# Optimization experiments

Measured on AMD Instinct MI355X. Metric: run time of the kernel, lower is better.

Reference implementation:

```python
import jax, jax.numpy as jnp
import numpy as np

MB, NK, DM, DT = 4096, 8, 1024, 128
EPS = 1e-3  # LayerNormalization eps, added to sigma OUTSIDE sqrt


def setup_inputs() -> dict:
    key = jax.random.key(0)
    ks = jax.random.split(key, 7)
    xav = lambda fan_in, fan_out: (2.0 / (fan_in + fan_out)) ** 0.5
    return {
        "q": jax.random.normal(ks[0], (MB, NK, DM), jnp.float32),
        "k": jax.random.normal(ks[1], (MB, NK, DM), jnp.float32),
        "v": jax.random.normal(ks[2], (MB, NK, DM), jnp.float32),
        "w_qs": jax.random.normal(ks[3], (NK, DM, DT), jnp.float32) * xav(DM, DT),
        "w_ks": jax.random.normal(ks[4], (NK, DM, DT), jnp.float32) * xav(DM, DT),
        "w_vs": jax.random.normal(ks[5], (NK, DM, DT), jnp.float32) * xav(DM, DT),
        # torch Linear: weight [out, in] = [NK*DM, NK*DT]
        "proj_w": jax.random.normal(ks[6], (NK * DM, NK * DT), jnp.float32) * xav(NK * DT, NK * DM),
        "proj_b": jnp.zeros((NK * DM,), jnp.float32),
        "gamma": jnp.ones((DM,), jnp.float32),
        "beta": jnp.zeros((DM,), jnp.float32),
    }


def reference(q, k, v, w_qs, w_ks, w_vs, proj_w, proj_b, gamma, beta):
    mb, nk, dm = q.shape
    dt = w_qs.shape[-1]
    residual = v

    # torch: q.view(n_kernel, mb, d_model) on contiguous [mb, nk, dm] == raw reshape
    q_s = jnp.einsum('nbd,ndt->nbt', q.reshape(nk, mb, dm), w_qs)  # [nk, mb, dt]
    k_s = jnp.einsum('nbd,ndt->nbt', k.reshape(nk, mb, dm), w_ks)
    v_s = jnp.einsum('nbd,ndt->nbt', v.reshape(nk, mb, dm), w_vs)

    # ScaledDotProductAttention on [nk*mb, 1, dt] -> scores [.,1,1]; softmax over
    # a singleton dim is identically 1, so output == v_s (faithful to source).
    temper = np.float32(np.sqrt(dm))
    scores = jnp.sum(q_s * k_s, axis=-1) / temper            # [nk, mb]
    attn = jax.nn.softmax(scores[:, :, None, None], axis=-1)  # [nk, mb, 1, 1] == 1.0
    out = attn[..., 0] * v_s                                  # [nk, mb, dt]
    attns = attn.reshape(nk * mb, 1, 1)

    # torch .view(mb, nk*dt) on the [nk, mb, dt]-contiguous buffer (raw reshape)
    outputs = out.reshape(mb, nk * dt)
    outputs = outputs @ proj_w.T + proj_b                     # [mb, nk*dm]
    z = outputs.reshape(mb, nk, dm) + residual

    # custom LayerNormalization: unbiased std, eps outside sqrt
    mu = jnp.mean(z, axis=-1, keepdims=True)
    sigma = jnp.std(z, axis=-1, keepdims=True, ddof=1)
    output = (z - mu) / (sigma + EPS) * gamma + beta
    return (output, attns)
```

## Files before the change

### kernel.cpp

```cpp
#include <hip/hip_runtime.h>
#include <cstdint>
#include <cstddef>

#define MB_   4096
#define NK_   8
#define DM_   1024
#define DT_   128

typedef __bf16 bf16;
typedef __bf16 bf16x8 __attribute__((ext_vector_type(8)));
typedef __bf16 bf16x4 __attribute__((ext_vector_type(4)));
typedef float  f32x4  __attribute__((ext_vector_type(4)));

__device__ __forceinline__ void gload_lds16(const void* g, void* l) {
  __builtin_amdgcn_global_load_lds(
      (__attribute__((address_space(1))) void*)g,
      (__attribute__((address_space(3))) void*)l,
      16, 0, 0);
}

__device__ __forceinline__ int hsw(int r) { return (r ^ (r >> 2)) & 3; }

__global__ void prep_kernel(const float* __restrict__ pw, bf16* __restrict__ pwb,
                            const float* __restrict__ wvs, bf16* __restrict__ wvt) {
  int b = blockIdx.x;
  if (b < 8192) {
    size_t i = ((size_t)b * 256 + threadIdx.x) * 4;
    float4 f = *(const float4*)&pw[i];
    bf16x4 o = { (bf16)f.x, (bf16)f.y, (bf16)f.z, (bf16)f.w };
    *(bf16x4*)&pwb[i] = o;
  } else {
    int o = (b - 8192) * 256 + threadIdx.x;
    int d = o & 1023;
    int t = (o >> 10) & 127;
    int n = o >> 17;
    wvt[o] = (bf16)wvs[(size_t)n * 131072 + (size_t)d * 128 + t];
  }
}

__global__ __launch_bounds__(256, 2) void gemm1_kernel(
    const float* __restrict__ vflat, const bf16* __restrict__ WvT,
    bf16* __restrict__ A2)
{
  __shared__ __align__(16) bf16 As[64 * 32];
  __shared__ __align__(16) bf16 Bs[128 * 32];
  const int tid  = threadIdx.x;
  const int wave = tid >> 6, lane = tid & 63;
  const int wm = wave >> 1, wn = wave & 1;
  const int n  = blockIdx.y;
  const int b0 = blockIdx.x * 64;

  const int r  = tid >> 2;
  const int hr = hsw(r);
  const int cs = (tid & 3) ^ hr;

  const float* ag = vflat + ((size_t)(n * MB_ + b0 + r)) * 1024 + (tid & 3) * 8;
  bf16* awr = As + r * 32 + cs * 8;
  const bf16* bg = WvT + (size_t)n * 131072 + (size_t)r * 1024 + cs * 8;
  char* bsb = (char*)Bs + wave * 1024;

  f32x4 acc[2][4] = {};
  const int krow = lane & 15;
  const int cch  = lane >> 4;
  const int swoff = ((cch ^ hsw(krow)) << 4);

  for (int kt = 0; kt < 32; ++kt) {
    const bf16* bptr = bg + kt * 32;
    gload_lds16(bptr,             bsb);
    gload_lds16(bptr + 64 * 1024, bsb + 4096);
    const float* aptr = ag + kt * 32;
    float4 f0 = *(const float4*)(aptr + 0);
    float4 f1 = *(const float4*)(aptr + 4);
    bf16x8 h0 = { (bf16)f0.x, (bf16)f0.y, (bf16)f0.z, (bf16)f0.w,
                  (bf16)f1.x, (bf16)f1.y, (bf16)f1.z, (bf16)f1.w };
    *(bf16x8*)awr = h0;
    __syncthreads();

    bf16x8 af[2], bfr[4];
    #pragma unroll
    for (int i = 0; i < 2; ++i)
      af[i] = *(const bf16x8*)((const char*)As + (wm * 32 + i * 16 + krow) * 64 + swoff);
    #pragma unroll
    for (int j = 0; j < 4; ++j)
      bfr[j] = *(const bf16x8*)((const char*)Bs + (wn * 64 + j * 16 + krow) * 64 + swoff);
    #pragma unroll
    for (int i = 0; i < 2; ++i)
      #pragma unroll
      for (int j = 0; j < 4; ++j)
        acc[i][j] = __builtin_amdgcn_mfma_f32_16x16x32_bf16(af[i], bfr[j], acc[i][j], 0, 0, 0);
    __syncthreads();
  }

  #pragma unroll
  for (int i = 0; i < 2; ++i) {
    #pragma unroll
    for (int j = 0; j < 4; ++j) {
      int t = wn * 64 + j * 16 + (lane & 15);
      #pragma unroll
      for (int rr = 0; rr < 4; ++rr) {
        int b = b0 + wm * 32 + i * 16 + (lane >> 4) * 4 + rr;
        size_t off = ((size_t)(n * 512 + (b >> 3))) * 1024 + (size_t)(b & 7) * 128 + t;
        A2[off] = (bf16)acc[i][j][rr];
      }
    }
  }
}

template<bool ZB>
__global__ __launch_bounds__(512, 2) void gemm2c_kernel(
    const bf16* __restrict__ A2, const bf16* __restrict__ PW,
    const float* __restrict__ pb, void* __restrict__ xoutp)
{
  __shared__ __align__(16) bf16 As[4][8192];
  __shared__ __align__(16) bf16 Bs[4][8192];

  const int tid  = threadIdx.x;
  const int w    = tid >> 6;
  const int lane = tid & 63;
  const int wm   = w >> 2;
  const int wn   = w & 3;

  const int bid   = blockIdx.x;
  const int x     = bid & 7;
  const int local = bid >> 3;
  const int mt    = local & 15;
  const int nt    = x * 4 + (local >> 4);
  const int m0    = mt * 256;
  const int n0    = nt * 256;

  const int rS = tid >> 2;
  const int cS = (tid & 3) ^ hsw(rS);
  const char* aG0 = (const char*)A2 + (size_t)(m0 + rS) * 2048 + cS * 16;
  const char* aG1 = aG0 + (size_t)128 * 2048;
  const char* bG0 = (const char*)PW + (size_t)(n0 + rS) * 2048 + cS * 16;
  const char* bG1 = bG0 + (size_t)128 * 2048;

  #define STAGE(t) { char* dA = (char*)As[(t) & 3] + tid * 16;               \
                     char* dB = (char*)Bs[(t) & 3] + tid * 16;               \
                     gload_lds16(aG0 + (size_t)(t) * 64, dA);                \
                     gload_lds16(aG1 + (size_t)(t) * 64, dA + 8192);         \
                     gload_lds16(bG0 + (size_t)(t) * 64, dB);                \
                     gload_lds16(bG1 + (size_t)(t) * 64, dB + 8192); }

  STAGE(0); STAGE(1); STAGE(2);
  asm volatile("s_waitcnt vmcnt(8)" ::: "memory");
  __builtin_amdgcn_s_barrier();
  __builtin_amdgcn_sched_barrier(0);

  f32x4 acc[8][4] = {};
  const int fr = lane & 15;
  const int g  = lane >> 4;
  const int swoff = ((g ^ hsw(fr)) << 4);
  const int aRd = (wm * 128 + fr) * 64 + swoff;
  const int bRd = (wn * 64  + fr) * 64 + swoff;

  #pragma unroll 1
  for (int s = 0; s < 32; ++s) {
    if (s < 29) STAGE(s + 3);

    const char* pA = (const char*)As[s & 3] + aRd;
    const char* pB = (const char*)Bs[s & 3] + bRd;
    bf16x8 a[8], b[4];
    #pragma unroll
    for (int m = 0; m < 8; ++m) a[m] = *(const bf16x8*)(pA + m * 1024);
    #pragma unroll
    for (int n = 0; n < 4; ++n) b[n] = *(const bf16x8*)(pB + n * 1024);
    #pragma unroll
    for (int m = 0; m < 8; ++m)
      #pragma unroll
      for (int n = 0; n < 4; ++n)
        acc[m][n] = __builtin_amdgcn_mfma_f32_16x16x32_bf16(a[m], b[n], acc[m][n], 0, 0, 0);

    asm volatile("s_waitcnt lgkmcnt(0)" ::: "memory");
    if (s < 29)       { asm volatile("s_waitcnt vmcnt(8)" ::: "memory"); }
    else if (s == 29) { asm volatile("s_waitcnt vmcnt(4)" ::: "memory"); }
    else if (s == 30) { asm volatile("s_waitcnt vmcnt(0)" ::: "memory"); }
    __builtin_amdgcn_s_barrier();
    __builtin_amdgcn_sched_barrier(0);
  }
  #undef STAGE

  #pragma unroll
  for (int m = 0; m < 8; ++m) {
    #pragma unroll
    for (int n = 0; n < 4; ++n) {
      int nn = n0 + wn * 64 + n * 16 + fr;
      float pbn = pb[nn];
      #pragma unroll
      for (int r = 0; r < 4; ++r) {
        int mm = m0 + wm * 128 + m * 16 + g * 4 + r;
        size_t off = (size_t)mm * 8192 + nn;
        float val = acc[m][n][r] + pbn;
        if (ZB) ((bf16*)xoutp)[off] = (bf16)val;
        else    ((float*)xoutp)[off] = val;
      }
    }
  }
}

template<bool ZB>
__global__ __launch_bounds__(256) void ln_kernel(
    const void* zin, const float* __restrict__ vres,
    const float* __restrict__ gamma, const float* __restrict__ beta,
    float* outp)
{
  __shared__ float red[16];
  const int row = blockIdx.x;
  const int tid = threadIdx.x;
  if (row < 128) outp[(size_t)33554432 + row * 256 + tid] = 1.0f;
  const size_t base = (size_t)row * 1024 + tid * 4;

  float4 rv = *(const float4*)&vres[base];
  float4 x;
  if (ZB) {
    bf16x4 zb4 = *(const bf16x4*)((const bf16*)zin + base);
    x.x = (float)zb4[0] + rv.x; x.y = (float)zb4[1] + rv.y;
    x.z = (float)zb4[2] + rv.z; x.w = (float)zb4[3] + rv.w;
  } else {
    float4 zf = *(const float4*)((const float*)zin + base);
    x.x = zf.x + rv.x; x.y = zf.y + rv.y; x.z = zf.z + rv.z; x.w = zf.w + rv.w;
  }

  float s  = x.x + x.y + x.z + x.w;
  float ss = x.x * x.x + x.y * x.y + x.z * x.z + x.w * x.w;
  #pragma unroll
  for (int m = 32; m >= 1; m >>= 1) {
    s  += __shfl_xor(s,  m, 64);
    ss += __shfl_xor(ss, m, 64);
  }
  const int wave = tid >> 6, lane = tid & 63;
  if (lane == 0) { red[wave] = s; red[wave + 8] = ss; }
  __syncthreads();
  float S  = red[0] + red[1] + red[2] + red[3];
  float SS = red[8] + red[9] + red[10] + red[11];
  float mu  = S * (1.0f / 1024.0f);
  float var = (SS - 1024.0f * mu * mu) * (1.0f / 1023.0f);
  var = var < 0.0f ? 0.0f : var;
  float rs = 1.0f / (sqrtf(var) + 1e-3f);
  float4 gmv = *(const float4*)&gamma[tid * 4];
  float4 be  = *(const float4*)&beta[tid * 4];
  float4 y;
  y.x = (x.x - mu) * rs * gmv.x + be.x;
  y.y = (x.y - mu) * rs * gmv.y + be.y;
  y.z = (x.z - mu) * rs * gmv.z + be.z;
  y.w = (x.w - mu) * rs * gmv.w + be.w;
  *(float4*)&outp[base] = y;
}

extern "C" void kernel_launch(void* const* d_in, const int* in_sizes, int n_in,
                              void* d_out, int out_size, void* d_ws, size_t ws_size,
                              hipStream_t stream) {
  const float* v     = (const float*)d_in[2];
  const float* wvs   = (const float*)d_in[5];
  const float* pw    = (const float*)d_in[6];
  const float* pb    = (const float*)d_in[7];
  const float* gamma = (const float*)d_in[8];
  const float* beta  = (const float*)d_in[9];
  float* out = (float*)d_out;

  const size_t OFF_WVT = 16777216;
  const size_t OFF_A2  = OFF_WVT + 2097152;
  const size_t OFF_X   = OFF_A2 + 8388608;
  const size_t NEED_ZB = OFF_X + 67108864;

  bf16* PWb = (bf16*)d_ws;
  bf16* WvT = (bf16*)((char*)d_ws + OFF_WVT);
  bf16* A2  = (bf16*)((char*)d_ws + OFF_A2);
  const bool zb = (ws_size >= NEED_ZB);
  void* xbuf = zb ? (void*)((char*)d_ws + OFF_X) : (void*)out;

  hipLaunchKernelGGL(prep_kernel, dim3(12288), dim3(256), 0, stream, pw, PWb, wvs, WvT);
  hipLaunchKernelGGL(gemm1_kernel, dim3(64, 8), dim3(256), 0, stream, v, WvT, A2);
  if (zb) {
    hipLaunchKernelGGL((gemm2c_kernel<true>),  dim3(512), dim3(512), 0, stream, A2, PWb, pb, xbuf);
    hipLaunchKernelGGL((ln_kernel<true>),      dim3(32768), dim3(256), 0, stream, xbuf, v, gamma, beta, out);
  } else {
    hipLaunchKernelGGL((gemm2c_kernel<false>), dim3(512), dim3(512), 0, stream, A2, PWb, pb, xbuf);
    hipLaunchKernelGGL((ln_kernel<false>),     dim3(32768), dim3(256), 0, stream, xbuf, v, gamma, beta, out);
  }
}
```

Measured before the change: 209.1 us.

## Use smaller 128x128 GEMM2 tiles and a bf16 residual copy for layernorm

Replaces the 256x256-tile, 512-thread projection GEMM with a 128x128-tile, 256-thread kernel using a 3-stage LDS pipeline and more blocks per CU. Separately, gemm1 writes a bf16 copy of v while it converts it, so the layernorm reads a 2-byte residual instead of fp32. Both aim to cut time, through better occupancy and through less layernorm read traffic. The costs are more re-reading of operands in GEMM2, an extra 64MB write in gemm1, and lower precision in the residual add. The bf16 residual is only used when the workspace is large enough.

```diff
diff --git a/kernel.cpp b/kernel.cpp
--- a/kernel.cpp
+++ b/kernel.cpp
@@ -38,9 +38,10 @@
   }
 }
 
+template<bool VB>
 __global__ __launch_bounds__(256, 2) void gemm1_kernel(
     const float* __restrict__ vflat, const bf16* __restrict__ WvT,
-    bf16* __restrict__ A2)
+    bf16* __restrict__ A2, bf16* __restrict__ vb)
 {
   __shared__ __align__(16) bf16 As[64 * 32];
   __shared__ __align__(16) bf16 Bs[128 * 32];
@@ -54,7 +55,8 @@
   const int hr = hsw(r);
   const int cs = (tid & 3) ^ hr;
 
-  const float* ag = vflat + ((size_t)(n * MB_ + b0 + r)) * 1024 + (tid & 3) * 8;
+  const size_t vbase = ((size_t)(n * MB_ + b0 + r)) * 1024 + (tid & 3) * 8;
+  const float* ag = vflat + vbase;
   bf16* awr = As + r * 32 + cs * 8;
   const bf16* bg = WvT + (size_t)n * 131072 + (size_t)r * 1024 + cs * 8;
   char* bsb = (char*)Bs + wave * 1024;
@@ -74,6 +76,7 @@
     bf16x8 h0 = { (bf16)f0.x, (bf16)f0.y, (bf16)f0.z, (bf16)f0.w,
                   (bf16)f1.x, (bf16)f1.y, (bf16)f1.z, (bf16)f1.w };
     *(bf16x8*)awr = h0;
+    if (VB) *(bf16x8*)&vb[vbase + kt * 32] = h0;
     __syncthreads();
 
     bf16x8 af[2], bfr[4];
@@ -107,90 +110,94 @@
 }
 
 template<bool ZB>
-__global__ __launch_bounds__(512, 2) void gemm2c_kernel(
+__global__ __launch_bounds__(256, 3) void gemm2k_kernel(
     const bf16* __restrict__ A2, const bf16* __restrict__ PW,
     const float* __restrict__ pb, void* __restrict__ xoutp)
 {
-  __shared__ __align__(16) bf16 As[4][8192];
-  __shared__ __align__(16) bf16 Bs[4][8192];
+  __shared__ __align__(16) bf16 As[3][4096];
+  __shared__ __align__(16) bf16 Bs[3][4096];
 
   const int tid  = threadIdx.x;
-  const int w    = tid >> 6;
-  const int lane = tid & 63;
-  const int wm   = w >> 2;
-  const int wn   = w & 3;
+  const int wave = tid >> 6, lane = tid & 63;
+  const int wm = wave >> 1, wn = wave & 1;
 
   const int bid   = blockIdx.x;
   const int x     = bid & 7;
   const int local = bid >> 3;
-  const int mt    = local & 15;
-  const int nt    = x * 4 + (local >> 4);
-  const int m0    = mt * 256;
-  const int n0    = nt * 256;
+  const int mt    = local & 31;
+  const int nt    = x * 8 + (local >> 5);
+  const int m0    = mt * 128;
+  const int n0    = nt * 128;
 
   const int rS = tid >> 2;
   const int cS = (tid & 3) ^ hsw(rS);
-  const char* aG0 = (const char*)A2 + (size_t)(m0 + rS) * 2048 + cS * 16;
-  const char* aG1 = aG0 + (size_t)128 * 2048;
-  const char* bG0 = (const char*)PW + (size_t)(n0 + rS) * 2048 + cS * 16;
-  const char* bG1 = bG0 + (size_t)128 * 2048;
-
-  #define STAGE(t) { char* dA = (char*)As[(t) & 3] + tid * 16;               \
-                     char* dB = (char*)Bs[(t) & 3] + tid * 16;               \
-                     gload_lds16(aG0 + (size_t)(t) * 64, dA);                \
-                     gload_lds16(aG1 + (size_t)(t) * 64, dA + 8192);         \
-                     gload_lds16(bG0 + (size_t)(t) * 64, dB);                \
-                     gload_lds16(bG1 + (size_t)(t) * 64, dB + 8192); }
-
-  STAGE(0); STAGE(1); STAGE(2);
-  asm volatile("s_waitcnt vmcnt(8)" ::: "memory");
+  const bf16* aG0 = A2 + (size_t)(m0 + rS) * 1024 + cS * 8;
+  const bf16* aG1 = aG0 + (size_t)64 * 1024;
+  const bf16* bG0 = PW + (size_t)(n0 + rS) * 1024 + cS * 8;
+  const bf16* bG1 = bG0 + (size_t)64 * 1024;
+  char* const ldsA = (char*)As[0] + wave * 1024;
+  char* const ldsB = (char*)Bs[0] + wave * 1024;
+
+  #define STAGE(t, bi) { char* dA = ldsA + (bi) * 8192;                      \
+                         char* dB = ldsB + (bi) * 8192;                      \
+                         gload_lds16(aG0 + (size_t)(t) * 32, dA);            \
+                         gload_lds16(aG1 + (size_t)(t) * 32, dA + 4096);     \
+                         gload_lds16(bG0 + (size_t)(t) * 32, dB);            \
+                         gload_lds16(bG1 + (size_t)(t) * 32, dB + 4096); }
+
+  STAGE(0, 0); STAGE(1, 1);
+  asm volatile("s_waitcnt vmcnt(4)" ::: "memory");
   __builtin_amdgcn_s_barrier();
   __builtin_amdgcn_sched_barrier(0);
 
-  f32x4 acc[8][4] = {};
-  const int fr = lane & 15;
-  const int g  = lane >> 4;
-  const int swoff = ((g ^ hsw(fr)) << 4);
-  const int aRd = (wm * 128 + fr) * 64 + swoff;
-  const int bRd = (wn * 64  + fr) * 64 + swoff;
-
+  f32x4 acc[4][4] = {};
+  const int krow = lane & 15;
+  const int cch  = lane >> 4;
+  const int swoff = ((cch ^ hsw(krow)) << 4);
+
+  int rd = 0;
   #pragma unroll 1
   for (int s = 0; s < 32; ++s) {
-    if (s < 29) STAGE(s + 3);
-
-    const char* pA = (const char*)As[s & 3] + aRd;
-    const char* pB = (const char*)Bs[s & 3] + bRd;
-    bf16x8 a[8], b[4];
-    #pragma unroll
-    for (int m = 0; m < 8; ++m) a[m] = *(const bf16x8*)(pA + m * 1024);
-    #pragma unroll
-    for (int n = 0; n < 4; ++n) b[n] = *(const bf16x8*)(pB + n * 1024);
-    #pragma unroll
-    for (int m = 0; m < 8; ++m)
+    const int st = rd >= 1 ? rd - 1 : 2;
+    if (s < 30) STAGE(s + 2, st);
+
+    const char* pA = (const char*)As[rd];
+    const char* pB = (const char*)Bs[rd];
+    bf16x8 af[4], bfr[4];
+    #pragma unroll
+    for (int i = 0; i < 4; ++i)
+      af[i] = *(const bf16x8*)(pA + (wm * 64 + i * 16 + krow) * 64 + swoff);
+    #pragma unroll
+    for (int j = 0; j < 4; ++j)
+      bfr[j] = *(const bf16x8*)(pB + (wn * 64 + j * 16 + krow) * 64 + swoff);
+    #pragma unroll
+    for (int i = 0; i < 4; ++i)
       #pragma unroll
-      for (int n = 0; n < 4; ++n)
-        acc[m][n] = __builtin_amdgcn_mfma_f32_16x16x32_bf16(a[m], b[n], acc[m][n], 0, 0, 0);
-
-    asm volatile("s_waitcnt lgkmcnt(0)" ::: "memory");
-    if (s < 29)       { asm volatile("s_waitcnt vmcnt(8)" ::: "memory"); }
-    else if (s == 29) { asm volatile("s_waitcnt vmcnt(4)" ::: "memory"); }
-    else if (s == 30) { asm volatile("s_waitcnt vmcnt(0)" ::: "memory"); }
-    __builtin_amdgcn_s_barrier();
-    __builtin_amdgcn_sched_barrier(0);
+      for (int j = 0; j < 4; ++j)
+        acc[i][j] = __builtin_amdgcn_mfma_f32_16x16x32_bf16(af[i], bfr[j], acc[i][j], 0, 0, 0);
+
+    if (s < 31) {
+      asm volatile("s_waitcnt lgkmcnt(0)" ::: "memory");
+      if (s < 30)       { asm volatile("s_waitcnt vmcnt(4)" ::: "memory"); }
+      else              { asm volatile("s_waitcnt vmcnt(0)" ::: "memory"); }
+      __builtin_amdgcn_s_barrier();
+      __builtin_amdgcn_sched_barrier(0);
+    }
+    rd = rd >= 2 ? 0 : rd + 1;
   }
   #undef STAGE
 
   #pragma unroll
-  for (int m = 0; m < 8; ++m) {
-    #pragma unroll
-    for (int n = 0; n < 4; ++n) {
-      int nn = n0 + wn * 64 + n * 16 + fr;
+  for (int i = 0; i < 4; ++i) {
+    #pragma unroll
+    for (int j = 0; j < 4; ++j) {
+      int nn = n0 + wn * 64 + j * 16 + krow;
       float pbn = pb[nn];
       #pragma unroll
       for (int r = 0; r < 4; ++r) {
-        int mm = m0 + wm * 128 + m * 16 + g * 4 + r;
+        int mm = m0 + wm * 64 + i * 16 + cch * 4 + r;
         size_t off = (size_t)mm * 8192 + nn;
-        float val = acc[m][n][r] + pbn;
+        float val = acc[i][j][r] + pbn;
         if (ZB) ((bf16*)xoutp)[off] = (bf16)val;
         else    ((float*)xoutp)[off] = val;
       }
@@ -198,9 +205,9 @@
   }
 }
 
-template<bool ZB>
+template<bool ZB, bool VB>
 __global__ __launch_bounds__(256) void ln_kernel(
-    const void* zin, const float* __restrict__ vres,
+    const void* zin, const float* __restrict__ vres, const bf16* __restrict__ vb,
     const float* __restrict__ gamma, const float* __restrict__ beta,
     float* outp)
 {
@@ -210,7 +217,13 @@
   if (row < 128) outp[(size_t)33554432 + row * 256 + tid] = 1.0f;
   const size_t base = (size_t)row * 1024 + tid * 4;
 
-  float4 rv = *(const float4*)&vres[base];
+  float4 rv;
+  if (VB) {
+    bf16x4 vb4 = *(const bf16x4*)(vb + base);
+    rv.x = (float)vb4[0]; rv.y = (float)vb4[1]; rv.z = (float)vb4[2]; rv.w = (float)vb4[3];
+  } else {
+    rv = *(const float4*)&vres[base];
+  }
   float4 x;
   if (ZB) {
     bf16x4 zb4 = *(const bf16x4*)((const bf16*)zin + base);
@@ -261,21 +274,32 @@
   const size_t OFF_WVT = 16777216;
   const size_t OFF_A2  = OFF_WVT + 2097152;
   const size_t OFF_X   = OFF_A2 + 8388608;
-  const size_t NEED_ZB = OFF_X + 67108864;
+  const size_t OFF_VB  = OFF_X + 67108864;
+  const size_t NEED_ZB = OFF_VB;
+  const size_t NEED_VB = OFF_VB + 67108864;
 
   bf16* PWb = (bf16*)d_ws;
   bf16* WvT = (bf16*)((char*)d_ws + OFF_WVT);
   bf16* A2  = (bf16*)((char*)d_ws + OFF_A2);
+  bf16* VB16= (bf16*)((char*)d_ws + OFF_VB);
   const bool zb = (ws_size >= NEED_ZB);
+  const bool vbe = (ws_size >= NEED_VB);
   void* xbuf = zb ? (void*)((char*)d_ws + OFF_X) : (void*)out;
 
   hipLaunchKernelGGL(prep_kernel, dim3(12288), dim3(256), 0, stream, pw, PWb, wvs, WvT);
-  hipLaunchKernelGGL(gemm1_kernel, dim3(64, 8), dim3(256), 0, stream, v, WvT, A2);
+  if (vbe)
+    hipLaunchKernelGGL((gemm1_kernel<true>),  dim3(64, 8), dim3(256), 0, stream, v, WvT, A2, VB16);
+  else
+    hipLaunchKernelGGL((gemm1_kernel<false>), dim3(64, 8), dim3(256), 0, stream, v, WvT, A2, VB16);
+
   if (zb) {
-    hipLaunchKernelGGL((gemm2c_kernel<true>),  dim3(512), dim3(512), 0, stream, A2, PWb, pb, xbuf);
-    hipLaunchKernelGGL((ln_kernel<true>),      dim3(32768), dim3(256), 0, stream, xbuf, v, gamma, beta, out);
+    hipLaunchKernelGGL((gemm2k_kernel<true>),  dim3(2048), dim3(256), 0, stream, A2, PWb, pb, xbuf);
+    if (vbe)
+      hipLaunchKernelGGL((ln_kernel<true, true>),  dim3(32768), dim3(256), 0, stream, xbuf, v, VB16, gamma, beta, out);
+    else
+      hipLaunchKernelGGL((ln_kernel<true, false>), dim3(32768), dim3(256), 0, stream, xbuf, v, VB16, gamma, beta, out);
   } else {
-    hipLaunchKernelGGL((gemm2c_kernel<false>), dim3(512), dim3(512), 0, stream, A2, PWb, pb, xbuf);
-    hipLaunchKernelGGL((ln_kernel<false>),     dim3(32768), dim3(256), 0, stream, xbuf, v, gamma, beta, out);
-  }
-}
+    hipLaunchKernelGGL((gemm2k_kernel<false>), dim3(2048), dim3(256), 0, stream, A2, PWb, pb, xbuf);
+    hipLaunchKernelGGL((ln_kernel<false, false>), dim3(32768), dim3(256), 0, stream, xbuf, v, VB16, gamma, beta, out);
+  }
+}
```

After: 230.5 us. 1.1x slower.
